# Performance work log

Measured on AMD Instinct MI355X. Metric: run time of the kernel, lower is better.

The kernel has to match this reference:

```python
import jax, jax.numpy as jnp
import numpy as np

D_MODEL = 1024
H = 16
DK = D_MODEL // H  # 64
BLK = 128
TAU = 1.0
EPS = 1e-12


def setup_inputs() -> dict:
    key = jax.random.key(0)
    ks = jax.random.split(key, 5)
    B, N = 1, 2048
    shp = (B, N, D_MODEL)
    q = jax.random.normal(ks[0], shp, dtype=jnp.float32)
    k = jax.random.normal(ks[1], shp, dtype=jnp.float32)
    v = jax.random.normal(ks[2], shp, dtype=jnp.float32)
    dO = jax.random.normal(ks[3], shp, dtype=jnp.float32)
    Tb = N // BLK  # 16 blocks per side
    block_sparse_mask = jax.random.randint(ks[4], (Tb, Tb), 0, 2, dtype=jnp.int32)
    return {"q": q, "k": k, "v": v, "dO": dO, "block_sparse_mask": block_sparse_mask}


def reference(q, k, v, dO, block_sparse_mask):
    B, N, _ = q.shape
    T = N // BLK  # number of blocks along sequence
    scale = TAU / np.sqrt(DK).astype(np.float32)

    def split(x):
        # (B,N,d_model) -> (B,H,T,BLK,DK)
        return x.reshape(B, N, H, DK).transpose(0, 2, 1, 3).reshape(B, H, T, BLK, DK)

    qb, kb, vb, dOb = split(q), split(k), split(v), split(dO)

    # block scores: (B,H,Ti,Tj,Br,Bc)
    S = jnp.einsum('bhipd,bhjqd->bhijpq', qb, kb) * scale
    # per-block (local) softmax normalization, exactly as in the source
    m = jnp.max(S, axis=-1, keepdims=True)
    P = jnp.exp(S - m)
    l = jnp.sum(P, axis=-1, keepdims=True)
    Pn = P / (l + EPS)

    dA = jnp.einsum('bhipd,bhjqd->bhijpq', dOb, vb)
    row_dot = jnp.sum(dA * Pn, axis=-1, keepdims=True)
    dS = Pn * (dA - row_dot)

    # block-sparse skipping: skipped (i,j) blocks contribute nothing
    bm = block_sparse_mask.astype(Pn.dtype)[None, None, :, :, None, None]
    Pn = Pn * bm
    dS = dS * bm

    dV = jnp.einsum('bhijpq,bhipd->bhjqd', Pn, dOb)
    dQ = jnp.einsum('bhijpq,bhjqd->bhipd', dS, kb) * scale
    dK = jnp.einsum('bhijpq,bhipd->bhjqd', dS, qb) * scale

    def merge(x):
        # (B,H,T,BLK,DK) -> (B,N,d_model)
        return x.reshape(B, H, N, DK).transpose(0, 2, 1, 3).reshape(B, N, D_MODEL)

    return (merge(dQ), merge(dK), merge(dV))
```

## Files before the change

### kernel.cpp

```cpp
#include <hip/hip_runtime.h>
#include <hip/hip_bf16.h>

#define DMODEL 1024
#define NHEAD  16
#define DKD    64
#define BLK    128
#define TB     16
#define SCALEF 0.125f

typedef __attribute__((ext_vector_type(8))) short bf16x8;
typedef __attribute__((ext_vector_type(4))) float f32x4;
typedef __attribute__((ext_vector_type(4))) unsigned int ui4;

#define MFMA(A, B, C) __builtin_amdgcn_mfma_f32_16x16x32_bf16(A, B, C, 0, 0, 0)

union U8 { bf16x8 v; ushort u[8]; ushort2 u2[4]; ushort4 u4[2]; };

__device__ __forceinline__ ushort2 pk2(float a, float b) {
  union { __hip_bfloat162 h; ushort2 u; } c;
  c.h = __float22bfloat162_rn(make_float2(a, b));
  return c.u;
}

__device__ __forceinline__ bf16x8 frag64(const ushort* T, int r, int c) {
  return *reinterpret_cast<const bf16x8*>(T + ((r * 64 + c) ^ ((r & 7) << 3)));
}
__device__ __forceinline__ bf16x8 frag64g(const ushort* T, int r, int c) {
  return __builtin_nontemporal_load(
      reinterpret_cast<const bf16x8*>(T + ((r * 64 + c) ^ ((r & 7) << 3))));
}
__device__ __forceinline__ bf16x8 frag128(const ushort* T, int r, int c) {
  return *reinterpret_cast<const bf16x8*>(T + ((r * 128 + c) ^ ((r & 7) << 3)));
}
__device__ __forceinline__ bf16x8 fragT2(const ushort* T, int d, int r0) {
  const int base = (r0 >> 2) * 256 + ((d * 4) ^ (((d >> 4) & 3) << 2));
  U8 x;
  x.u4[0] = *reinterpret_cast<const ushort4*>(T + base);
  x.u4[1] = *reinterpret_cast<const ushort4*>(T + base + 256);
  return x.v;
}
__device__ __forceinline__ bf16x8 gfrag(const float* __restrict__ g, float sc) {
  const float4 fa = *reinterpret_cast<const float4*>(g);
  const float4 fb = *reinterpret_cast<const float4*>(g + 4);
  U8 x;
  x.u2[0] = pk2(fa.x * sc, fa.y * sc);
  x.u2[1] = pk2(fa.z * sc, fa.w * sc);
  x.u2[2] = pk2(fb.x * sc, fb.y * sc);
  x.u2[3] = pk2(fb.z * sc, fb.w * sc);
  return x.v;
}

__device__ __forceinline__ void gwrow(ushort* T, const float* __restrict__ g,
                                      float sc, int tid) {
#pragma unroll
  for (int it = 0; it < 4; ++it) {
    const int idx = tid + 512 * it;
    const int r = idx >> 4, d4 = idx & 15;
    const float4 f = *reinterpret_cast<const float4*>(g + r * DMODEL + 4 * d4);
    const ushort2 lo = pk2(f.x * sc, f.y * sc);
    const ushort2 hi = pk2(f.z * sc, f.w * sc);
    ushort4 u; u.x = lo.x; u.y = lo.y; u.z = hi.x; u.w = hi.y;
    *reinterpret_cast<ushort4*>(T + ((r * 64 + 4 * d4) ^ ((r & 7) << 3))) = u;
  }
}
__device__ __forceinline__ void gwchunk(ushort* T, const float* __restrict__ g,
                                        float sc, int tid) {
  const int a = (tid >> 4) & 3;
#pragma unroll
  for (int it = 0; it < 4; ++it) {
    const int idx = tid + 512 * it;
    const int r = idx >> 4, d4 = idx & 15;
    const float4 f = *reinterpret_cast<const float4*>(g + r * DMODEL + 4 * d4);
    const float w0 = f.x * sc, w1 = f.y * sc, w2 = f.z * sc, w3 = f.w * sc;
    const float s0 = __shfl_xor(w1, 16), s1 = __shfl_xor(w0, 16);
    const float s2 = __shfl_xor(w3, 16), s3 = __shfl_xor(w2, 16);
    const float u0 = (a & 1) ? s0 : w0;
    const float u1 = (a & 1) ? w1 : s1;
    const float u2 = (a & 1) ? s2 : w2;
    const float u3 = (a & 1) ? w3 : s3;
    const float t0 = __shfl_xor(u2, 32), t1 = __shfl_xor(u3, 32);
    const float t2 = __shfl_xor(u0, 32), t3 = __shfl_xor(u1, 32);
    const float z0 = (a & 2) ? t0 : u0;
    const float z1 = (a & 2) ? t1 : u1;
    const float z2 = (a & 2) ? u2 : t2;
    const float z3 = (a & 2) ? u3 : t3;
    const int d = 4 * d4 + a, R0 = r - a;
    const ushort2 lo = pk2(z0, z1);
    const ushort2 hi = pk2(z2, z3);
    ushort4 o; o.x = lo.x; o.y = lo.y; o.z = hi.x; o.w = hi.y;
    *reinterpret_cast<ushort4*>(T + (R0 >> 2) * 256 + ((d * 4) ^ (((d >> 4) & 3) << 2))) = o;
  }
}

__device__ __forceinline__ ushort* IMGp(ushort* ws, int imgN, int h, int t, int i) {
  return ws + (((size_t)h * TB + t) * imgN + i) * 8192;
}
__device__ __forceinline__ const ushort* IMGc(const ushort* ws, int imgN, int h, int t, int i) {
  return ws + (((size_t)h * TB + t) * imgN + i) * 8192;
}

__global__ void __launch_bounds__(512, 2)
prepass(const float* __restrict__ q, const float* __restrict__ kk,
        const float* __restrict__ v, const float* __restrict__ dOg,
        ushort* __restrict__ ws, int imgN) {
  const int bid = blockIdx.x;
  const int h = bid >> 4, t = bid & 15;
  const int tid = threadIdx.x;
  const size_t off = (size_t)(t * BLK) * DMODEL + h * DKD;
  gwrow  (IMGp(ws, imgN, h, t, 0), kk + off, SCALEF, tid);
  gwrow  (IMGp(ws, imgN, h, t, 1), v  + off, 1.f,    tid);
  gwchunk(IMGp(ws, imgN, h, t, 2), kk + off, SCALEF, tid);
  gwchunk(IMGp(ws, imgN, h, t, 3), q  + off, SCALEF, tid);
  gwchunk(IMGp(ws, imgN, h, t, 4), dOg + off, 1.f,   tid);
  if (imgN >= 7) {
    gwrow(IMGp(ws, imgN, h, t, 5), q   + off, 1.f, tid);
    gwrow(IMGp(ws, imgN, h, t, 6), dOg + off, 1.f, tid);
  }
}

__device__ __forceinline__ void nt_issue(const ushort* src, int tid, ui4* r) {
  const ui4* s = reinterpret_cast<const ui4*>(src);
  r[0] = __builtin_nontemporal_load(s + tid);
  r[1] = __builtin_nontemporal_load(s + tid + 512);
}
__device__ __forceinline__ void lds_wr(ushort* dst, const ui4* r, int tid) {
  ui4* d = reinterpret_cast<ui4*>(dst);
  d[tid] = r[0];
  d[tid + 512] = r[1];
}

__global__ void __launch_bounds__(512, 2)
bwd_roles(const float* __restrict__ q, const float* __restrict__ dOg,
          const ushort* __restrict__ ws, const int* __restrict__ mask, int imgN,
          float* __restrict__ dQ, float* __restrict__ dK, float* __restrict__ dV) {
  __shared__ ushort sm[65536];
  ushort* X = sm + 49152;
  const int tid = threadIdx.x;
  const int l = tid & 63, l15 = l & 15, lg = (l >> 4) & 3;
  const int w = tid >> 6, pw = w * 16;
  const int bid = blockIdx.x;
  const int xcd = bid & 7, idx = bid >> 3;
  const int h    = (xcd << 1) | (idx & 1);
  const int role = (idx >> 1) & 1;
  const int blk  = (idx >> 2) & 15;
  const f32x4 zz = {0.f, 0.f, 0.f, 0.f};

  if (role == 0) {
    unsigned bm = 0;
    for (int t = 0; t < TB; ++t)
      if (mask[blk * TB + t]) bm |= 1u << t;

    bf16x8 bq[2], bo[2];
#pragma unroll
    for (int kb = 0; kb < 2; ++kb) {
      const size_t row = (size_t)(blk * BLK + pw + l15) * DMODEL + h * DKD + kb * 32 + lg * 8;
      bq[kb] = gfrag(q + row, 1.f);
      bo[kb] = gfrag(dOg + row, 1.f);
    }
    f32x4 accQ[4] = {zz, zz, zz, zz};

    if (bm) {
      int j = __ffs(bm) - 1;
      unsigned rest = bm & (bm - 1);
      {
        ui4 t0[2], t1[2], t2[2];
        nt_issue(IMGc(ws, imgN, h, j, 0), tid, t0);
        nt_issue(IMGc(ws, imgN, h, j, 1), tid, t1);
        nt_issue(IMGc(ws, imgN, h, j, 2), tid, t2);
        lds_wr(sm + 0, t0, tid);
        lds_wr(sm + 8192, t1, tid);
        lds_wr(sm + 16384, t2, tid);
      }
      __syncthreads();
      int cur = 0;
      while (j >= 0) {
        const int jn = rest ? (__ffs(rest) - 1) : -1;
        rest = rest ? (rest & (rest - 1)) : 0u;
        ui4 pk0[2], pk1[2], pk2r[2];
        if (jn >= 0) {
          nt_issue(IMGc(ws, imgN, h, jn, 0), tid, pk0);
          nt_issue(IMGc(ws, imgN, h, jn, 1), tid, pk1);
          nt_issue(IMGc(ws, imgN, h, jn, 2), tid, pk2r);
        }
        const ushort* kR = sm + cur * 24576;
        const ushort* vR = sm + cur * 24576 + 8192;
        const ushort* kT = sm + cur * 24576 + 16384;

        f32x4 ST[8], dAT[8];
#pragma unroll
        for (int mf = 0; mf < 8; ++mf) { ST[mf] = zz; dAT[mf] = zz; }
#pragma unroll
        for (int kb = 0; kb < 2; ++kb) {
          const int ck = kb * 32 + lg * 8;
#pragma unroll
          for (int mf = 0; mf < 8; ++mf) {
            ST[mf]  = MFMA(frag64(kR, mf * 16 + l15, ck), bq[kb], ST[mf]);
            dAT[mf] = MFMA(frag64(vR, mf * 16 + l15, ck), bo[kb], dAT[mf]);
          }
        }
        float mx = -1e30f;
#pragma unroll
        for (int mf = 0; mf < 8; ++mf)
#pragma unroll
          for (int r = 0; r < 4; ++r) mx = fmaxf(mx, ST[mf][r]);
        mx = fmaxf(mx, __shfl_xor(mx, 16));
        mx = fmaxf(mx, __shfl_xor(mx, 32));
        float ss = 0.f;
#pragma unroll
        for (int mf = 0; mf < 8; ++mf)
#pragma unroll
          for (int r = 0; r < 4; ++r) { const float e = __expf(ST[mf][r] - mx); ST[mf][r] = e; ss += e; }
        ss += __shfl_xor(ss, 16);
        ss += __shfl_xor(ss, 32);
        const float inv = 1.f / (ss + 1e-12f);
        float rd = 0.f;
#pragma unroll
        for (int mf = 0; mf < 8; ++mf)
#pragma unroll
          for (int r = 0; r < 4; ++r) { const float pn = ST[mf][r] * inv; ST[mf][r] = pn; rd += pn * dAT[mf][r]; }
        rd += __shfl_xor(rd, 16);
        rd += __shfl_xor(rd, 32);
#pragma unroll
        for (int mf = 0; mf < 8; ++mf)
#pragma unroll
          for (int r = 0; r < 4; ++r) dAT[mf][r] = ST[mf][r] * (dAT[mf][r] - rd);

        const int p = pw + l15;
#pragma unroll
        for (int mf = 0; mf < 8; ++mf) {
          const ushort2 lo = pk2(dAT[mf][0], dAT[mf][1]);
          const ushort2 hi = pk2(dAT[mf][2], dAT[mf][3]);
          ushort4 u; u.x = lo.x; u.y = lo.y; u.z = hi.x; u.w = hi.y;
          *reinterpret_cast<ushort4*>(X + ((p * 128 + mf * 16 + 4 * lg) ^ ((p & 7) << 3))) = u;
        }
        __syncthreads();

#pragma unroll
        for (int kc = 0; kc < 4; ++kc) {
          const int cc = kc * 32 + lg * 8;
          const bf16x8 a = frag128(X, pw + l15, cc);
#pragma unroll
          for (int nfd = 0; nfd < 4; ++nfd)
            accQ[nfd] = MFMA(a, fragT2(kT, nfd * 16 + l15, cc), accQ[nfd]);
        }
        if (jn >= 0) {
          ushort* nb = sm + (cur ^ 1) * 24576;
          lds_wr(nb, pk0, tid);
          lds_wr(nb + 8192, pk1, tid);
          lds_wr(nb + 16384, pk2r, tid);
        }
        __syncthreads();
        cur ^= 1;
        j = jn;
      }
    }
#pragma unroll
    for (int nfd = 0; nfd < 4; ++nfd)
#pragma unroll
      for (int r = 0; r < 4; ++r)
        __builtin_nontemporal_store(accQ[nfd][r],
            &dQ[(size_t)(blk * BLK + pw + lg * 4 + r) * DMODEL + h * DKD + nfd * 16 + l15]);

  } else {
    const int jb = blk;
    unsigned bm = 0;
    for (int t = 0; t < TB; ++t)
      if (mask[t * TB + jb]) bm |= 1u << t;

    f32x4 accK[4] = {zz, zz, zz, zz};
    f32x4 accV[4] = {zz, zz, zz, zz};

    if (bm) {
      const bool hasR = (imgN >= 7);
      int i = __ffs(bm) - 1;
      unsigned rest = bm & (bm - 1);
      bf16x8 aq[2], ao[2];
      {
        ui4 t0[2], t1[2], t2[2], t3[2];
        nt_issue(IMGc(ws, imgN, h, jb, 0), tid, t0);
        nt_issue(IMGc(ws, imgN, h, jb, 1), tid, t1);
        nt_issue(IMGc(ws, imgN, h, i, 3), tid, t2);
        nt_issue(IMGc(ws, imgN, h, i, 4), tid, t3);
        lds_wr(sm + 0, t0, tid);
        lds_wr(sm + 8192, t1, tid);
        lds_wr(sm + 16384, t2, tid);
        lds_wr(sm + 32768, t3, tid);
        if (hasR) {
#pragma unroll
          for (int kb = 0; kb < 2; ++kb) {
            aq[kb] = frag64g(IMGc(ws, imgN, h, i, 5), pw + l15, kb * 32 + lg * 8);
            ao[kb] = frag64g(IMGc(ws, imgN, h, i, 6), pw + l15, kb * 32 + lg * 8);
          }
        } else {
#pragma unroll
          for (int kb = 0; kb < 2; ++kb) {
            const size_t row = (size_t)(i * BLK + pw + l15) * DMODEL + h * DKD + kb * 32 + lg * 8;
            aq[kb] = gfrag(q + row, 1.f);
            ao[kb] = gfrag(dOg + row, 1.f);
          }
        }
      }
      __syncthreads();
      const ushort* kR = sm;
      const ushort* vR = sm + 8192;
      int cur = 0;
      while (i >= 0) {
        const int in = rest ? (__ffs(rest) - 1) : -1;
        rest = rest ? (rest & (rest - 1)) : 0u;
        ui4 pq[2], po[2];
        bf16x8 nq[2], no[2];
        if (in >= 0) {
          nt_issue(IMGc(ws, imgN, h, in, 3), tid, pq);
          nt_issue(IMGc(ws, imgN, h, in, 4), tid, po);
          if (hasR) {
#pragma unroll
            for (int kb = 0; kb < 2; ++kb) {
              nq[kb] = frag64g(IMGc(ws, imgN, h, in, 5), pw + l15, kb * 32 + lg * 8);
              no[kb] = frag64g(IMGc(ws, imgN, h, in, 6), pw + l15, kb * 32 + lg * 8);
            }
          } else {
#pragma unroll
            for (int kb = 0; kb < 2; ++kb) {
              const size_t row = (size_t)(in * BLK + pw + l15) * DMODEL + h * DKD + kb * 32 + lg * 8;
              nq[kb] = gfrag(q + row, 1.f);
              no[kb] = gfrag(dOg + row, 1.f);
            }
          }
        }
        const ushort* qT = sm + 16384 + cur * 8192;
        const ushort* oT = sm + 32768 + cur * 8192;

        f32x4 S[8], dA[8];
#pragma unroll
        for (int nf = 0; nf < 8; ++nf) { S[nf] = zz; dA[nf] = zz; }
#pragma unroll
        for (int kb = 0; kb < 2; ++kb) {
          const int ck = kb * 32 + lg * 8;
#pragma unroll
          for (int nf = 0; nf < 8; ++nf) {
            S[nf]  = MFMA(aq[kb], frag64(kR, nf * 16 + l15, ck), S[nf]);
            dA[nf] = MFMA(ao[kb], frag64(vR, nf * 16 + l15, ck), dA[nf]);
          }
        }
#pragma unroll
        for (int r = 0; r < 4; ++r) {
          float mx = -1e30f;
#pragma unroll
          for (int nf = 0; nf < 8; ++nf) mx = fmaxf(mx, S[nf][r]);
          mx = fmaxf(mx, __shfl_xor(mx, 1));
          mx = fmaxf(mx, __shfl_xor(mx, 2));
          mx = fmaxf(mx, __shfl_xor(mx, 4));
          mx = fmaxf(mx, __shfl_xor(mx, 8));
          float ss = 0.f;
#pragma unroll
          for (int nf = 0; nf < 8; ++nf) { const float e = __expf(S[nf][r] - mx); S[nf][r] = e; ss += e; }
          ss += __shfl_xor(ss, 1); ss += __shfl_xor(ss, 2);
          ss += __shfl_xor(ss, 4); ss += __shfl_xor(ss, 8);
          const float inv = 1.f / (ss + 1e-12f);
          float rd = 0.f;
#pragma unroll
          for (int nf = 0; nf < 8; ++nf) { const float pn = S[nf][r] * inv; S[nf][r] = pn; rd += pn * dA[nf][r]; }
          rd += __shfl_xor(rd, 1); rd += __shfl_xor(rd, 2);
          rd += __shfl_xor(rd, 4); rd += __shfl_xor(rd, 8);
#pragma unroll
          for (int nf = 0; nf < 8; ++nf) dA[nf][r] = S[nf][r] * (dA[nf][r] - rd);
        }

#pragma unroll
        for (int nf = 0; nf < 8; ++nf) {
          const int c = nf * 16 + l15;
          const ushort2 lo = pk2(S[nf][0], S[nf][1]);
          const ushort2 hi = pk2(S[nf][2], S[nf][3]);
          ushort4 u; u.x = lo.x; u.y = lo.y; u.z = hi.x; u.w = hi.y;
          *reinterpret_cast<ushort4*>(X + ((c * 128 + pw + 4 * lg) ^ ((c & 7) << 3))) = u;
        }
        __syncthreads();

#pragma unroll
        for (int kp = 0; kp < 4; ++kp) {
          const int pp = kp * 32 + lg * 8;
          const bf16x8 a = frag128(X, pw + l15, pp);
#pragma unroll
          for (int nfd = 0; nfd < 4; ++nfd)
            accV[nfd] = MFMA(a, fragT2(oT, nfd * 16 + l15, pp), accV[nfd]);
        }
        __syncthreads();

#pragma unroll
        for (int nf = 0; nf < 8; ++nf) {
          const int c = nf * 16 + l15;
          const ushort2 lo = pk2(dA[nf][0], dA[nf][1]);
          const ushort2 hi = pk2(dA[nf][2], dA[nf][3]);
          ushort4 u; u.x = lo.x; u.y = lo.y; u.z = hi.x; u.w = hi.y;
          *reinterpret_cast<ushort4*>(X + ((c * 128 + pw + 4 * lg) ^ ((c & 7) << 3))) = u;
        }
        __syncthreads();

#pragma unroll
        for (int kp = 0; kp < 4; ++kp) {
          const int pp = kp * 32 + lg * 8;
          const bf16x8 a = frag128(X, pw + l15, pp);
#pragma unroll
          for (int nfd = 0; nfd < 4; ++nfd)
            accK[nfd] = MFMA(a, fragT2(qT, nfd * 16 + l15, pp), accK[nfd]);
        }
        if (in >= 0) {
          lds_wr(sm + 16384 + (cur ^ 1) * 8192, pq, tid);
          lds_wr(sm + 32768 + (cur ^ 1) * 8192, po, tid);
          aq[0] = nq[0]; aq[1] = nq[1];
          ao[0] = no[0]; ao[1] = no[1];
        }
        __syncthreads();
        cur ^= 1;
        i = in;
      }
    }
#pragma unroll
    for (int nfd = 0; nfd < 4; ++nfd)
#pragma unroll
      for (int r = 0; r < 4; ++r) {
        const size_t rowo = (size_t)(jb * BLK + pw + lg * 4 + r) * DMODEL + h * DKD + nfd * 16 + l15;
        __builtin_nontemporal_store(accK[nfd][r], &dK[rowo]);
        __builtin_nontemporal_store(accV[nfd][r], &dV[rowo]);
      }
  }
}

extern "C" void kernel_launch(void* const* d_in, const int* in_sizes, int n_in,
                              void* d_out, int out_size, void* d_ws, size_t ws_size,
                              hipStream_t stream) {
  const float* q  = (const float*)d_in[0];
  const float* k  = (const float*)d_in[1];
  const float* v  = (const float*)d_in[2];
  const float* dO = (const float*)d_in[3];
  const int* mask = (const int*)d_in[4];
  float* out = (float*)d_out;
  float* dQ = out;
  float* dK = out + (size_t)2048 * DMODEL;
  float* dV = out + (size_t)2 * 2048 * DMODEL;
  ushort* ws = (ushort*)d_ws;

  const size_t need7 = (size_t)NHEAD * TB * 7 * 16384;
  const int imgN = (ws_size >= need7) ? 7 : 5;

  prepass<<<NHEAD * TB, 512, 0, stream>>>(q, k, v, dO, ws, imgN);
  bwd_roles<<<2 * NHEAD * TB, 512, 0, stream>>>(q, dO, ws, mask, imgN, dQ, dK, dV);
}
```

Before: 120.4 us.

## Compute dQ from registers with fp16 MFMA and merge dK/dV LDS passes

The dQ role now feeds the dS^T fragments straight from registers as fp16 operands into 16x16x16 f16 MFMAs against an fp16 K-chunk image, removing an LDS round-trip and a barrier per block. The dK/dV role writes Pn and dS into two separate LDS buffers in one pass and runs both accumulations in one loop, dropping two barriers. It also drops the double-buffered Q/dO tiles and sets launch bounds to one block per CU. In exchange, fp16 replaces bf16 for dS and the scaled K in the dQ path, so out-of-range values could overflow. Single buffering may expose load latency, and lower occupancy may hide latency less well.

Measured after the change: 119.7 us. No clear change (-0.6%).

```diff
diff --git a/kernel.cpp b/kernel.cpp
--- a/kernel.cpp
+++ b/kernel.cpp
@@ -9,10 +9,12 @@
 #define SCALEF 0.125f
 
 typedef __attribute__((ext_vector_type(8))) short bf16x8;
+typedef __attribute__((ext_vector_type(4))) _Float16 f16x4;
 typedef __attribute__((ext_vector_type(4))) float f32x4;
 typedef __attribute__((ext_vector_type(4))) unsigned int ui4;
 
-#define MFMA(A, B, C) __builtin_amdgcn_mfma_f32_16x16x32_bf16(A, B, C, 0, 0, 0)
+#define MFMA(A, B, C)   __builtin_amdgcn_mfma_f32_16x16x32_bf16(A, B, C, 0, 0, 0)
+#define MFMA16(A, B, C) __builtin_amdgcn_mfma_f32_16x16x16f16(A, B, C, 0, 0, 0)
 
 union U8 { bf16x8 v; ushort u[8]; ushort2 u2[4]; ushort4 u4[2]; };
 
@@ -20,6 +22,12 @@
   union { __hip_bfloat162 h; ushort2 u; } c;
   c.h = __float22bfloat162_rn(make_float2(a, b));
   return c.u;
+}
+__device__ __forceinline__ ushort4 pkh4(float a, float b, float c, float d) {
+  union { f16x4 h; ushort4 u; } z;
+  z.h[0] = (_Float16)a; z.h[1] = (_Float16)b;
+  z.h[2] = (_Float16)c; z.h[3] = (_Float16)d;
+  return z.u;
 }
 
 __device__ __forceinline__ bf16x8 frag64(const ushort* T, int r, int c) {
@@ -38,6 +46,11 @@
   x.u4[0] = *reinterpret_cast<const ushort4*>(T + base);
   x.u4[1] = *reinterpret_cast<const ushort4*>(T + base + 256);
   return x.v;
+}
+__device__ __forceinline__ f16x4 fragK16(const ushort* T, int d, int g) {
+  union { ushort4 u; f16x4 h; } z;
+  z.u = *reinterpret_cast<const ushort4*>(T + g * 256 + ((d * 4) ^ (((d >> 4) & 3) << 2)));
+  return z.h;
 }
 __device__ __forceinline__ bf16x8 gfrag(const float* __restrict__ g, float sc) {
   const float4 fa = *reinterpret_cast<const float4*>(g);
@@ -63,6 +76,7 @@
     *reinterpret_cast<ushort4*>(T + ((r * 64 + 4 * d4) ^ ((r & 7) << 3))) = u;
   }
 }
+template <int HALF>
 __device__ __forceinline__ void gwchunk(ushort* T, const float* __restrict__ g,
                                         float sc, int tid) {
   const int a = (tid >> 4) & 3;
@@ -85,9 +99,14 @@
     const float z2 = (a & 2) ? u2 : t2;
     const float z3 = (a & 2) ? u3 : t3;
     const int d = 4 * d4 + a, R0 = r - a;
-    const ushort2 lo = pk2(z0, z1);
-    const ushort2 hi = pk2(z2, z3);
-    ushort4 o; o.x = lo.x; o.y = lo.y; o.z = hi.x; o.w = hi.y;
+    ushort4 o;
+    if constexpr (HALF) {
+      o = pkh4(z0, z1, z2, z3);
+    } else {
+      const ushort2 lo = pk2(z0, z1);
+      const ushort2 hi = pk2(z2, z3);
+      o.x = lo.x; o.y = lo.y; o.z = hi.x; o.w = hi.y;
+    }
     *reinterpret_cast<ushort4*>(T + (R0 >> 2) * 256 + ((d * 4) ^ (((d >> 4) & 3) << 2))) = o;
   }
 }
@@ -107,11 +126,11 @@
   const int h = bid >> 4, t = bid & 15;
   const int tid = threadIdx.x;
   const size_t off = (size_t)(t * BLK) * DMODEL + h * DKD;
-  gwrow  (IMGp(ws, imgN, h, t, 0), kk + off, SCALEF, tid);
-  gwrow  (IMGp(ws, imgN, h, t, 1), v  + off, 1.f,    tid);
-  gwchunk(IMGp(ws, imgN, h, t, 2), kk + off, SCALEF, tid);
-  gwchunk(IMGp(ws, imgN, h, t, 3), q  + off, SCALEF, tid);
-  gwchunk(IMGp(ws, imgN, h, t, 4), dOg + off, 1.f,   tid);
+  gwrow     (IMGp(ws, imgN, h, t, 0), kk + off, SCALEF, tid);
+  gwrow     (IMGp(ws, imgN, h, t, 1), v  + off, 1.f,    tid);
+  gwchunk<1>(IMGp(ws, imgN, h, t, 2), kk + off, SCALEF, tid);
+  gwchunk<0>(IMGp(ws, imgN, h, t, 3), q  + off, SCALEF, tid);
+  gwchunk<0>(IMGp(ws, imgN, h, t, 4), dOg + off, 1.f,   tid);
   if (imgN >= 7) {
     gwrow(IMGp(ws, imgN, h, t, 5), q   + off, 1.f, tid);
     gwrow(IMGp(ws, imgN, h, t, 6), dOg + off, 1.f, tid);
@@ -129,12 +148,11 @@
   d[tid + 512] = r[1];
 }
 
-__global__ void __launch_bounds__(512, 2)
+__global__ void __launch_bounds__(512, 1)
 bwd_roles(const float* __restrict__ q, const float* __restrict__ dOg,
           const ushort* __restrict__ ws, const int* __restrict__ mask, int imgN,
           float* __restrict__ dQ, float* __restrict__ dK, float* __restrict__ dV) {
   __shared__ ushort sm[65536];
-  ushort* X = sm + 49152;
   const int tid = threadIdx.x;
   const int l = tid & 63, l15 = l & 15, lg = (l >> 4) & 3;
   const int w = tid >> 6, pw = w * 16;
@@ -157,7 +175,7 @@
       bq[kb] = gfrag(q + row, 1.f);
       bo[kb] = gfrag(dOg + row, 1.f);
     }
-    f32x4 accQ[4] = {zz, zz, zz, zz};
+    f32x4 accQT[4] = {zz, zz, zz, zz};
 
     if (bm) {
       int j = __ffs(bm) - 1;
@@ -220,29 +238,20 @@
           for (int r = 0; r < 4; ++r) { const float pn = ST[mf][r] * inv; ST[mf][r] = pn; rd += pn * dAT[mf][r]; }
         rd += __shfl_xor(rd, 16);
         rd += __shfl_xor(rd, 32);
-#pragma unroll
-        for (int mf = 0; mf < 8; ++mf)
-#pragma unroll
-          for (int r = 0; r < 4; ++r) dAT[mf][r] = ST[mf][r] * (dAT[mf][r] - rd);
-
-        const int p = pw + l15;
+
+        f16x4 pb[8];
 #pragma unroll
         for (int mf = 0; mf < 8; ++mf) {
-          const ushort2 lo = pk2(dAT[mf][0], dAT[mf][1]);
-          const ushort2 hi = pk2(dAT[mf][2], dAT[mf][3]);
-          ushort4 u; u.x = lo.x; u.y = lo.y; u.z = hi.x; u.w = hi.y;
-          *reinterpret_cast<ushort4*>(X + ((p * 128 + mf * 16 + 4 * lg) ^ ((p & 7) << 3))) = u;
-        }
-        __syncthreads();
-
-#pragma unroll
-        for (int kc = 0; kc < 4; ++kc) {
-          const int cc = kc * 32 + lg * 8;
-          const bf16x8 a = frag128(X, pw + l15, cc);
-#pragma unroll
-          for (int nfd = 0; nfd < 4; ++nfd)
-            accQ[nfd] = MFMA(a, fragT2(kT, nfd * 16 + l15, cc), accQ[nfd]);
-        }
+#pragma unroll
+          for (int r = 0; r < 4; ++r)
+            pb[mf][r] = (_Float16)(ST[mf][r] * (dAT[mf][r] - rd));
+        }
+#pragma unroll
+        for (int df = 0; df < 4; ++df)
+#pragma unroll
+          for (int mf = 0; mf < 8; ++mf)
+            accQT[df] = MFMA16(fragK16(kT, df * 16 + l15, mf * 4 + lg), pb[mf], accQT[df]);
+
         if (jn >= 0) {
           ushort* nb = sm + (cur ^ 1) * 24576;
           lds_wr(nb, pk0, tid);
@@ -255,11 +264,13 @@
       }
     }
 #pragma unroll
-    for (int nfd = 0; nfd < 4; ++nfd)
-#pragma unroll
-      for (int r = 0; r < 4; ++r)
-        __builtin_nontemporal_store(accQ[nfd][r],
-            &dQ[(size_t)(blk * BLK + pw + lg * 4 + r) * DMODEL + h * DKD + nfd * 16 + l15]);
+    for (int df = 0; df < 4; ++df) {
+      f32x4 wv;
+      wv[0] = accQT[df][0]; wv[1] = accQT[df][1];
+      wv[2] = accQT[df][2]; wv[3] = accQT[df][3];
+      __builtin_nontemporal_store(wv, reinterpret_cast<f32x4*>(
+          dQ + (size_t)(blk * BLK + pw + l15) * DMODEL + h * DKD + df * 16 + lg * 4));
+    }
 
   } else {
     const int jb = blk;
@@ -272,6 +283,12 @@
 
     if (bm) {
       const bool hasR = (imgN >= 7);
+      ushort* kR = sm;
+      ushort* vR = sm + 8192;
+      ushort* qT = sm + 16384;
+      ushort* oT = sm + 24576;
+      ushort* X1 = sm + 32768;
+      ushort* X2 = sm + 49152;
       int i = __ffs(bm) - 1;
       unsigned rest = bm & (bm - 1);
       bf16x8 aq[2], ao[2];
@@ -281,10 +298,10 @@
         nt_issue(IMGc(ws, imgN, h, jb, 1), tid, t1);
         nt_issue(IMGc(ws, imgN, h, i, 3), tid, t2);
         nt_issue(IMGc(ws, imgN, h, i, 4), tid, t3);
-        lds_wr(sm + 0, t0, tid);
-        lds_wr(sm + 8192, t1, tid);
-        lds_wr(sm + 16384, t2, tid);
-        lds_wr(sm + 32768, t3, tid);
+        lds_wr(kR, t0, tid);
+        lds_wr(vR, t1, tid);
+        lds_wr(qT, t2, tid);
+        lds_wr(oT, t3, tid);
         if (hasR) {
 #pragma unroll
           for (int kb = 0; kb < 2; ++kb) {
@@ -301,9 +318,7 @@
         }
       }
       __syncthreads();
-      const ushort* kR = sm;
-      const ushort* vR = sm + 8192;
-      int cur = 0;
+
       while (i >= 0) {
         const int in = rest ? (__ffs(rest) - 1) : -1;
         rest = rest ? (rest & (rest - 1)) : 0u;
@@ -327,8 +342,6 @@
             }
           }
         }
-        const ushort* qT = sm + 16384 + cur * 8192;
-        const ushort* oT = sm + 32768 + cur * 8192;
 
         f32x4 S[8], dA[8];
 #pragma unroll
@@ -369,49 +382,41 @@
 #pragma unroll
         for (int nf = 0; nf < 8; ++nf) {
           const int c = nf * 16 + l15;
-          const ushort2 lo = pk2(S[nf][0], S[nf][1]);
-          const ushort2 hi = pk2(S[nf][2], S[nf][3]);
-          ushort4 u; u.x = lo.x; u.y = lo.y; u.z = hi.x; u.w = hi.y;
-          *reinterpret_cast<ushort4*>(X + ((c * 128 + pw + 4 * lg) ^ ((c & 7) << 3))) = u;
+          const int off = (c * 128 + pw + 4 * lg) ^ ((c & 7) << 3);
+          {
+            const ushort2 lo = pk2(S[nf][0], S[nf][1]);
+            const ushort2 hi = pk2(S[nf][2], S[nf][3]);
+            ushort4 u; u.x = lo.x; u.y = lo.y; u.z = hi.x; u.w = hi.y;
+            *reinterpret_cast<ushort4*>(X1 + off) = u;
+          }
+          {
+            const ushort2 lo = pk2(dA[nf][0], dA[nf][1]);
+            const ushort2 hi = pk2(dA[nf][2], dA[nf][3]);
+            ushort4 u; u.x = lo.x; u.y = lo.y; u.z = hi.x; u.w = hi.y;
+            *reinterpret_cast<ushort4*>(X2 + off) = u;
+          }
         }
         __syncthreads();
 
 #pragma unroll
         for (int kp = 0; kp < 4; ++kp) {
           const int pp = kp * 32 + lg * 8;
-          const bf16x8 a = frag128(X, pw + l15, pp);
-#pragma unroll
-          for (int nfd = 0; nfd < 4; ++nfd)
-            accV[nfd] = MFMA(a, fragT2(oT, nfd * 16 + l15, pp), accV[nfd]);
+          const bf16x8 a1 = frag128(X1, pw + l15, pp);
+          const bf16x8 a2 = frag128(X2, pw + l15, pp);
+#pragma unroll
+          for (int nfd = 0; nfd < 4; ++nfd) {
+            accV[nfd] = MFMA(a1, fragT2(oT, nfd * 16 + l15, pp), accV[nfd]);
+            accK[nfd] = MFMA(a2, fragT2(qT, nfd * 16 + l15, pp), accK[nfd]);
+          }
         }
         __syncthreads();
 
-#pragma unroll
-        for (int nf = 0; nf < 8; ++nf) {
-          const int c = nf * 16 + l15;
-          const ushort2 lo = pk2(dA[nf][0], dA[nf][1]);
-          const ushort2 hi = pk2(dA[nf][2], dA[nf][3]);
-          ushort4 u; u.x = lo.x; u.y = lo.y; u.z = hi.x; u.w = hi.y;
-          *reinterpret_cast<ushort4*>(X + ((c * 128 + pw + 4 * lg) ^ ((c & 7) << 3))) = u;
-        }
-        __syncthreads();
-
-#pragma unroll
-        for (int kp = 0; kp < 4; ++kp) {
-          const int pp = kp * 32 + lg * 8;
-          const bf16x8 a = frag128(X, pw + l15, pp);
-#pragma unroll
-          for (int nfd = 0; nfd < 4; ++nfd)
-            accK[nfd] = MFMA(a, fragT2(qT, nfd * 16 + l15, pp), accK[nfd]);
-        }
         if (in >= 0) {
-          lds_wr(sm + 16384 + (cur ^ 1) * 8192, pq, tid);
-          lds_wr(sm + 32768 + (cur ^ 1) * 8192, po, tid);
+          lds_wr(qT, pq, tid);
+          lds_wr(oT, po, tid);
           aq[0] = nq[0]; aq[1] = nq[1];
           ao[0] = no[0]; ao[1] = no[1];
         }
-        __syncthreads();
-        cur ^= 1;
         i = in;
       }
     }
```
